# Optimization experiments

Measured on AMD Instinct MI355X. Metric: run time of the kernel, lower is better.

The kernel has to match this reference:

```python
import jax, jax.numpy as jnp
import numpy as np
import math

B, H, L, D = 8, 16, 1024, 64


def setup_inputs() -> dict:
    key = jax.random.key(0)
    kq, kk, kv, kb, km = jax.random.split(key, 5)
    q = jax.random.normal(kq, (B, H, L, D), dtype=jnp.float32)
    k = jax.random.normal(kk, (B, H, L, D), dtype=jnp.float32)
    v = jax.random.normal(kv, (B, H, L, D), dtype=jnp.float32)
    bias = jax.random.uniform(kb, (B, 1, L, L), dtype=jnp.float32)
    mask = jax.random.randint(km, (B, 1, L, L), 0, 2, dtype=jnp.int32)
    return {"q": q, "k": k, "v": v, "bias": bias, "mask": mask}


def reference(q, k, v, bias, mask):
    d_tensor = q.shape[-1]
    # score = q @ k^T / sqrt(d)  -> [B,H,L,L]
    score = jnp.einsum('bhqd,bhkd->bhqk', q, k) / math.sqrt(d_tensor)
    score = score * bias                      # multiplicative bias
    score = jnp.where(mask == 0, jnp.float32(-10000.0), score)  # masked_fill
    score = jax.nn.softmax(score, axis=-1)
    out = jnp.einsum('bhqk,bhkd->bhqd', score, v)
    return (out, score)
```

## Files before the change

kernel.cpp:

```cpp
#include <hip/hip_runtime.h>
#include <math.h>

typedef _Float16 f16x8 __attribute__((ext_vector_type(8)));
typedef _Float16 f16x4 __attribute__((ext_vector_type(4)));
typedef float f32x4 __attribute__((ext_vector_type(4)));

#define MFMA16(a, b, c) __builtin_amdgcn_mfma_f32_16x16x32_f16(a, b, c, 0, 0, 0)

constexpr int L = 1024;
constexpr int D = 64;
constexpr int BH = 128;
constexpr size_t OUT_ELEMS = 8ull * 16 * 1024 * 64;
constexpr size_t PLANE = (size_t)BH * L * D;
constexpr size_t BMN   = 8ull * 1024 * 1024;

__device__ __forceinline__ int swzh(int row, int col) {
    return row * L + (col ^ ((row & 7) << 3));
}

__global__ __launch_bounds__(256)
void prep_all(const float* __restrict__ kg, const float* __restrict__ vg,
              const float* __restrict__ bias, const int* __restrict__ mask,
              _Float16* __restrict__ kf, _Float16* __restrict__ vtf,
              _Float16* __restrict__ bmp) {
    __shared__ __align__(16) char smem[16640];
    const int bid = blockIdx.x;
    const int tid = threadIdx.x;

    if (bid < 4096) {
        const size_t t = ((size_t)bid * 256 + tid) * 8;
        float4 a0 = *(const float4*)(kg + t);
        float4 a1 = *(const float4*)(kg + t + 4);
        f16x8 o;
        o[0] = (_Float16)(0.125f * a0.x); o[1] = (_Float16)(0.125f * a0.y);
        o[2] = (_Float16)(0.125f * a0.z); o[3] = (_Float16)(0.125f * a0.w);
        o[4] = (_Float16)(0.125f * a1.x); o[5] = (_Float16)(0.125f * a1.y);
        o[6] = (_Float16)(0.125f * a1.z); o[7] = (_Float16)(0.125f * a1.w);
        *(f16x8*)(kf + t) = o;
    } else if (bid < 6144) {
        _Float16 (*tile)[72] = (_Float16(*)[72])smem;
        const int vb = bid - 4096;
        const int bh = vb >> 4;
        const int k0 = (vb & 15) * 64;
#pragma unroll
        for (int r = 0; r < 4; ++r) {
            const int k  = r * 16 + (tid >> 4);
            const int d0 = (tid & 15) * 4;
            float4 a = *(const float4*)(vg + ((size_t)(bh * L + k0 + k)) * D + d0);
            tile[d0 + 0][k] = (_Float16)a.x;
            tile[d0 + 1][k] = (_Float16)a.y;
            tile[d0 + 2][k] = (_Float16)a.z;
            tile[d0 + 3][k] = (_Float16)a.w;
        }
        __syncthreads();
#pragma unroll
        for (int w = 0; w < 4; ++w) {
            const int d   = w * 16 + (tid >> 4);
            const int kk0 = (tid & 15) * 4;
            const size_t dst = (size_t)bh * (D * L) + (size_t)d * L + k0 + kk0;
            *(f16x4*)(vtf + dst) = *(const f16x4*)&tile[d][kk0];
        }
    } else {
        float (*tile)[132] = (float(*)[132])smem;
        const int wgid = bid - 6144;
        const int w    = wgid & 7;
        const int bqt  = wgid >> 3;
        const int qt = bqt & 31;
        const int b  = bqt >> 5;
        _Float16* outr = bmp + (size_t)wgid * 4096;
#pragma unroll 1
        for (int half = 0; half < 2; ++half) {
            const size_t rowbase = ((size_t)b * L + qt * 32 + half * 16) * L + w * 128;
#pragma unroll
            for (int h = 0; h < 8; ++h) {
                const int idx = h * 256 + tid;
                const int row = idx >> 7, col = idx & 127;
                float bv = bias[rowbase + (size_t)row * L + col];
                int   mv = mask[rowbase + (size_t)row * L + col];
                tile[row][col] = mv ? bv : -1.0f;
            }
            __syncthreads();
            const int lam = tid & 63;
            const int lr = lam & 15, lg = lam >> 4;
            const int g = tid >> 6;
            f16x8 o;
#pragma unroll
            for (int s = 0; s < 8; ++s) {
                const int slot = g * 8 + s;
                const int ct = slot >> 2, r = slot & 3;
                o[s] = (_Float16)tile[lr][ct * 16 + 4 * lg + r];
            }
            *(f16x8*)(outr + half * 2048 + (size_t)tid * 8) = o;
            __syncthreads();
        }
    }
}

__global__ __launch_bounds__(512, 4)
void attn_main(const float* __restrict__ qg, const _Float16* __restrict__ kf_g,
               const _Float16* __restrict__ vtf_g, const _Float16* __restrict__ bmp_g,
               float* __restrict__ outg) {
    __shared__ __align__(16) _Float16 plds[32 * L];
    float* red = (float*)plds;

    const int wg = (blockIdx.x & 7) * 512 + (blockIdx.x >> 3);
    const int bh = wg >> 5;
    const int qt = wg & 31;
    const int b  = bh >> 4;
    const int q0 = qt * 32;
    const int tid  = threadIdx.x;
    const int wave = tid >> 6;
    const int lane = tid & 63;
    const int lg   = lane >> 4;
    const int lr   = lane & 15;

    const float*    qp = qg + (size_t)bh * L * D;
    const _Float16* kp = kf_g + (size_t)bh * L * D;
    const int kbase = wave * 128;

    f16x8 qf[2][2];
#pragma unroll
    for (int t = 0; t < 2; ++t) {
        const float* src = qp + (size_t)(q0 + t * 16 + lr) * D + lg * 8;
        float4 a0 = *(const float4*)src;
        float4 a1 = *(const float4*)(src + 4);
        float4 a2 = *(const float4*)(src + 32);
        float4 a3 = *(const float4*)(src + 36);
        qf[t][0][0] = (_Float16)a0.x; qf[t][0][1] = (_Float16)a0.y;
        qf[t][0][2] = (_Float16)a0.z; qf[t][0][3] = (_Float16)a0.w;
        qf[t][0][4] = (_Float16)a1.x; qf[t][0][5] = (_Float16)a1.y;
        qf[t][0][6] = (_Float16)a1.z; qf[t][0][7] = (_Float16)a1.w;
        qf[t][1][0] = (_Float16)a2.x; qf[t][1][1] = (_Float16)a2.y;
        qf[t][1][2] = (_Float16)a2.z; qf[t][1][3] = (_Float16)a2.w;
        qf[t][1][4] = (_Float16)a3.x; qf[t][1][5] = (_Float16)a3.y;
        qf[t][1][6] = (_Float16)a3.z; qf[t][1][7] = (_Float16)a3.w;
    }

    f32x4 acc[2][8];
#pragma unroll
    for (int ct = 0; ct < 8; ++ct) {
        const _Float16* krow = kp + (size_t)(kbase + ct * 16 + lr) * D + lg * 8;
        f16x8 kv0 = *(const f16x8*)(krow);
        f16x8 kv1 = *(const f16x8*)(krow + 32);
#pragma unroll
        for (int t = 0; t < 2; ++t) {
            f32x4 a = {0.f, 0.f, 0.f, 0.f};
            a = MFMA16(kv0, qf[t][0], a);
            a = MFMA16(kv1, qf[t][1], a);
            acc[t][ct] = a;
        }
    }

    const _Float16* bmr = bmp_g + ((size_t)(b * 32 + qt) * 8 + wave) * 4096;
#pragma unroll
    for (int t = 0; t < 2; ++t) {
#pragma unroll
        for (int g = 0; g < 4; ++g) {
            f16x8 bv = *(const f16x8*)(bmr + t * 2048 + g * 512 + lane * 8);
#pragma unroll
            for (int s = 0; s < 8; ++s) {
                const int slot = g * 8 + s;
                float tt = (float)bv[s];
                float a = acc[t][slot >> 2][slot & 3];
                acc[t][slot >> 2][slot & 3] = (tt >= 0.f) ? a * tt : -INFINITY;
            }
        }
    }

    float m[2], ls[2];
#pragma unroll
    for (int t = 0; t < 2; ++t) m[t] = -INFINITY;
#pragma unroll
    for (int ct = 0; ct < 8; ++ct)
#pragma unroll
        for (int t = 0; t < 2; ++t)
#pragma unroll
            for (int r = 0; r < 4; ++r) m[t] = fmaxf(m[t], acc[t][ct][r]);
#pragma unroll
    for (int t = 0; t < 2; ++t) {
        m[t] = fmaxf(m[t], __shfl_xor(m[t], 16));
        m[t] = fmaxf(m[t], __shfl_xor(m[t], 32));
        m[t] = fmaxf(m[t], -10000.0f);
        ls[t] = 0.f;
    }
#pragma unroll
    for (int ct = 0; ct < 8; ++ct)
#pragma unroll
        for (int t = 0; t < 2; ++t)
#pragma unroll
            for (int r = 0; r < 4; ++r) {
                float p = __expf(acc[t][ct][r] - m[t]);
                acc[t][ct][r] = p;
                ls[t] += p;
            }
#pragma unroll
    for (int t = 0; t < 2; ++t) {
        ls[t] += __shfl_xor(ls[t], 16);
        ls[t] += __shfl_xor(ls[t], 32);
    }

    if (lg == 0) {
#pragma unroll
        for (int t = 0; t < 2; ++t) {
            red[(wave * 32 + t * 16 + lr) * 2 + 0] = m[t];
            red[(wave * 32 + t * 16 + lr) * 2 + 1] = ls[t];
        }
    }
    __syncthreads();

    float scale[2];
#pragma unroll
    for (int t = 0; t < 2; ++t) {
        const int row = t * 16 + lr;
        float M = -INFINITY;
#pragma unroll
        for (int w = 0; w < 8; ++w) M = fmaxf(M, red[(w * 32 + row) * 2]);
        float denom = 0.f;
#pragma unroll
        for (int w = 0; w < 8; ++w)
            denom += red[(w * 32 + row) * 2 + 1] * __expf(red[(w * 32 + row) * 2] - M);
        denom = fmaxf(denom, 1e-37f);
        scale[t] = __expf(m[t] - M) / denom;
    }
    __syncthreads();

#pragma unroll
    for (int t = 0; t < 2; ++t)
#pragma unroll
        for (int ct = 0; ct < 8; ++ct) {
            f16x4 pv;
#pragma unroll
            for (int r = 0; r < 4; ++r) pv[r] = (_Float16)(acc[t][ct][r] * scale[t]);
            *(f16x4*)&plds[swzh(t * 16 + lr, kbase + ct * 16 + 4 * lg)] = pv;
        }
    __syncthreads();

    const int row0 = wave * 4;
    float* srow0 = outg + OUT_ELEMS + (size_t)bh * L * L + (size_t)(q0 + row0) * L;
#pragma unroll
    for (int rr = 0; rr < 4; ++rr) {
#pragma unroll
        for (int mt = 0; mt < 4; ++mt) {
            const int col = mt * 256 + lane * 4;
            f16x4 pv = *(const f16x4*)&plds[swzh(row0 + rr, col)];
            f32x4 o = {(float)pv[0], (float)pv[1], (float)pv[2], (float)pv[3]};
            *(f32x4*)(srow0 + (size_t)rr * L + col) = o;
        }
    }

    const int qsub = wave >> 2;
    const int d0   = (wave & 3) * 16;
    const _Float16* vrow = vtf_g + (size_t)bh * D * L + (size_t)(d0 + lr) * L;
    f32x4 oacc = {0.f, 0.f, 0.f, 0.f};
#pragma unroll
    for (int kb = 0; kb < L; kb += 32) {
        const int e0 = kb + lg * 8;
        f16x8 pa = *(const f16x8*)&plds[swzh(qsub * 16 + lr, e0)];
        f16x8 vb = *(const f16x8*)(vrow + e0);
        oacc = MFMA16(pa, vb, oacc);
    }
#pragma unroll
    for (int r = 0; r < 4; ++r) {
        outg[((size_t)bh * L + q0 + qsub * 16 + lg * 4 + r) * D + d0 + lr] = oacc[r];
    }
}

extern "C" void kernel_launch(void* const* d_in, const int* in_sizes, int n_in,
                              void* d_out, int out_size, void* d_ws, size_t ws_size,
                              hipStream_t stream) {
    const float* q    = (const float*)d_in[0];
    const float* k    = (const float*)d_in[1];
    const float* v    = (const float*)d_in[2];
    const float* bias = (const float*)d_in[3];
    const int*   mask = (const int*)d_in[4];
    float* out = (float*)d_out;

    const size_t need = (2 * PLANE + BMN) * sizeof(_Float16);
    if (ws_size < need) return;

    _Float16* kf  = (_Float16*)d_ws;
    _Float16* vtf = kf + PLANE;
    _Float16* bmp = vtf + PLANE;

    hipLaunchKernelGGL(prep_all, dim3(8192), dim3(256), 0, stream,
                       k, v, bias, mask, kf, vtf, bmp);
    hipLaunchKernelGGL(attn_main, dim3(4096), dim3(512), 0, stream,
                       q, kf, vtf, bmp, out);
}
```

Measured before the change: 338.7 us.

## Fuse bias/mask preprocessing into attention kernel, read fp32 bias and int mask directly

```diff
diff --git a/kernel.cpp b/kernel.cpp
--- a/kernel.cpp
+++ b/kernel.cpp
@@ -12,18 +12,15 @@
 constexpr int BH = 128;
 constexpr size_t OUT_ELEMS = 8ull * 16 * 1024 * 64;
 constexpr size_t PLANE = (size_t)BH * L * D;
-constexpr size_t BMN   = 8ull * 1024 * 1024;
 
 __device__ __forceinline__ int swzh(int row, int col) {
     return row * L + (col ^ ((row & 7) << 3));
 }
 
 __global__ __launch_bounds__(256)
-void prep_all(const float* __restrict__ kg, const float* __restrict__ vg,
-              const float* __restrict__ bias, const int* __restrict__ mask,
-              _Float16* __restrict__ kf, _Float16* __restrict__ vtf,
-              _Float16* __restrict__ bmp) {
-    __shared__ __align__(16) char smem[16640];
+void prep_kv(const float* __restrict__ kg, const float* __restrict__ vg,
+             _Float16* __restrict__ kf, _Float16* __restrict__ vtf) {
+    __shared__ __align__(16) _Float16 tile[64][72];
     const int bid = blockIdx.x;
     const int tid = threadIdx.x;
 
@@ -37,8 +34,7 @@
         o[4] = (_Float16)(0.125f * a1.x); o[5] = (_Float16)(0.125f * a1.y);
         o[6] = (_Float16)(0.125f * a1.z); o[7] = (_Float16)(0.125f * a1.w);
         *(f16x8*)(kf + t) = o;
-    } else if (bid < 6144) {
-        _Float16 (*tile)[72] = (_Float16(*)[72])smem;
+    } else {
         const int vb = bid - 4096;
         const int bh = vb >> 4;
         const int k0 = (vb & 15) * 64;
@@ -60,46 +56,13 @@
             const size_t dst = (size_t)bh * (D * L) + (size_t)d * L + k0 + kk0;
             *(f16x4*)(vtf + dst) = *(const f16x4*)&tile[d][kk0];
         }
-    } else {
-        float (*tile)[132] = (float(*)[132])smem;
-        const int wgid = bid - 6144;
-        const int w    = wgid & 7;
-        const int bqt  = wgid >> 3;
-        const int qt = bqt & 31;
-        const int b  = bqt >> 5;
-        _Float16* outr = bmp + (size_t)wgid * 4096;
-#pragma unroll 1
-        for (int half = 0; half < 2; ++half) {
-            const size_t rowbase = ((size_t)b * L + qt * 32 + half * 16) * L + w * 128;
-#pragma unroll
-            for (int h = 0; h < 8; ++h) {
-                const int idx = h * 256 + tid;
-                const int row = idx >> 7, col = idx & 127;
-                float bv = bias[rowbase + (size_t)row * L + col];
-                int   mv = mask[rowbase + (size_t)row * L + col];
-                tile[row][col] = mv ? bv : -1.0f;
-            }
-            __syncthreads();
-            const int lam = tid & 63;
-            const int lr = lam & 15, lg = lam >> 4;
-            const int g = tid >> 6;
-            f16x8 o;
-#pragma unroll
-            for (int s = 0; s < 8; ++s) {
-                const int slot = g * 8 + s;
-                const int ct = slot >> 2, r = slot & 3;
-                o[s] = (_Float16)tile[lr][ct * 16 + 4 * lg + r];
-            }
-            *(f16x8*)(outr + half * 2048 + (size_t)tid * 8) = o;
-            __syncthreads();
-        }
     }
 }
 
 __global__ __launch_bounds__(512, 4)
 void attn_main(const float* __restrict__ qg, const _Float16* __restrict__ kf_g,
-               const _Float16* __restrict__ vtf_g, const _Float16* __restrict__ bmp_g,
-               float* __restrict__ outg) {
+               const _Float16* __restrict__ vtf_g, const float* __restrict__ biasg,
+               const int* __restrict__ maskg, float* __restrict__ outg) {
     __shared__ __align__(16) _Float16 plds[32 * L];
     float* red = (float*)plds;
 
@@ -117,6 +80,11 @@
     const float*    qp = qg + (size_t)bh * L * D;
     const _Float16* kp = kf_g + (size_t)bh * L * D;
     const int kbase = wave * 128;
+
+    const float* brow0 = biasg + (size_t)b * L * L + (size_t)(q0 + lr) * L + kbase + lg * 4;
+    const float* brow1 = brow0 + 16 * L;
+    const int*   mrow0 = maskg + (size_t)b * L * L + (size_t)(q0 + lr) * L + kbase + lg * 4;
+    const int*   mrow1 = mrow0 + 16 * L;
 
     f16x8 qf[2][2];
 #pragma unroll
@@ -142,28 +110,22 @@
         const _Float16* krow = kp + (size_t)(kbase + ct * 16 + lr) * D + lg * 8;
         f16x8 kv0 = *(const f16x8*)(krow);
         f16x8 kv1 = *(const f16x8*)(krow + 32);
+        float4 bv0 = *(const float4*)(brow0 + ct * 16);
+        float4 bv1 = *(const float4*)(brow1 + ct * 16);
+        int4   mv0 = *(const int4*)(mrow0 + ct * 16);
+        int4   mv1 = *(const int4*)(mrow1 + ct * 16);
 #pragma unroll
         for (int t = 0; t < 2; ++t) {
             f32x4 a = {0.f, 0.f, 0.f, 0.f};
             a = MFMA16(kv0, qf[t][0], a);
             a = MFMA16(kv1, qf[t][1], a);
+            const float4 bv = t ? bv1 : bv0;
+            const int4   mv = t ? mv1 : mv0;
+            a[0] = mv.x ? a[0] * bv.x : -INFINITY;
+            a[1] = mv.y ? a[1] * bv.y : -INFINITY;
+            a[2] = mv.z ? a[2] * bv.z : -INFINITY;
+            a[3] = mv.w ? a[3] * bv.w : -INFINITY;
             acc[t][ct] = a;
-        }
-    }
-
-    const _Float16* bmr = bmp_g + ((size_t)(b * 32 + qt) * 8 + wave) * 4096;
-#pragma unroll
-    for (int t = 0; t < 2; ++t) {
-#pragma unroll
-        for (int g = 0; g < 4; ++g) {
-            f16x8 bv = *(const f16x8*)(bmr + t * 2048 + g * 512 + lane * 8);
-#pragma unroll
-            for (int s = 0; s < 8; ++s) {
-                const int slot = g * 8 + s;
-                float tt = (float)bv[s];
-                float a = acc[t][slot >> 2][slot & 3];
-                acc[t][slot >> 2][slot & 3] = (tt >= 0.f) ? a * tt : -INFINITY;
-            }
         }
     }
 
@@ -275,15 +237,13 @@
     const int*   mask = (const int*)d_in[4];
     float* out = (float*)d_out;
 
-    const size_t need = (2 * PLANE + BMN) * sizeof(_Float16);
+    const size_t need = 2 * PLANE * sizeof(_Float16);
     if (ws_size < need) return;
 
     _Float16* kf  = (_Float16*)d_ws;
     _Float16* vtf = kf + PLANE;
-    _Float16* bmp = vtf + PLANE;
-
-    hipLaunchKernelGGL(prep_all, dim3(8192), dim3(256), 0, stream,
-                       k, v, bias, mask, kf, vtf, bmp);
+
+    hipLaunchKernelGGL(prep_kv, dim3(6144), dim3(256), 0, stream, k, v, kf, vtf);
     hipLaunchKernelGGL(attn_main, dim3(4096), dim3(512), 0, stream,
-                       q, kf, vtf, bmp, out);
-}
+                       q, kf, vtf, bias, mask, out);
+}
```

After: 434.1 us. 28.2% more time.
